# Kernel tuning notes

Measured on AMD Instinct MI355X. Metric: run time of the kernel, lower is better.

## Reference

```python
import jax, jax.numpy as jnp
import numpy as np

# dims
BB, T, D_IN = 16, 2048, 64
D = 512          # hidden_dim (d_model)
DI = 2 * D       # d_inner (expand=2)
N = 16           # d_state
DC = 4           # d_conv
R = D // 16      # dt_rank = 32
L = 3            # n_layer
D_OUT = 128


def setup_inputs() -> dict:
    key = jax.random.key(0)
    ks = jax.random.split(key, 10)
    g = lambda k, shape, s: (jax.random.normal(k, shape, jnp.float32) * s)
    A_log = jnp.tile(jnp.log(jnp.arange(1, N + 1, dtype=jnp.float32))[None, None, :], (L, DI, 1))
    return {
        "x": g(ks[0], (BB, T, D_IN), 1.0),
        "Wi": g(ks[1], (D, D_IN), 0.05), "bi": jnp.zeros((D,), jnp.float32),
        "Win": g(ks[2], (L, 2 * DI, D), 0.02),
        "convw": g(ks[3], (L, DI, DC), 0.2), "convb": jnp.zeros((L, DI), jnp.float32),
        "Wx": g(ks[4], (L, R + 2 * N, DI), 0.02),
        "Wdt": g(ks[5], (L, DI, R), 0.05), "bdt": jnp.full((L, DI), -1.0, jnp.float32),
        "A_log": A_log, "Dp": jnp.ones((L, DI), jnp.float32),
        "Wout": g(ks[6], (L, D, DI), 0.02),
        "Wo": g(ks[7], (D_OUT, D), 0.05), "bo": jnp.zeros((D_OUT,), jnp.float32),
    }


def _selective_scan(u, delta, A, Bm, Cm, Dv):
    # u, delta: [B,T,DI]; A: [DI,N]; Bm, Cm: [B,T,N]; Dv: [DI]
    def step(h, inp):
        d_t, u_t, B_t, C_t = inp  # [B,DI],[B,DI],[B,N],[B,N]
        dA = jnp.exp(d_t[:, :, None] * A)                      # [B,DI,N]
        h = dA * h + (d_t * u_t)[:, :, None] * B_t[:, None, :]  # [B,DI,N]
        y = jnp.einsum('bdn,bn->bd', h, C_t)
        return h, y

    h0 = jnp.zeros((u.shape[0], u.shape[2], A.shape[1]), u.dtype)
    xs = (delta.transpose(1, 0, 2), u.transpose(1, 0, 2),
          Bm.transpose(1, 0, 2), Cm.transpose(1, 0, 2))
    _, ys = jax.lax.scan(step, h0, xs)
    return ys.transpose(1, 0, 2) + u * Dv


def _mamba_layer(x, Win, cw, cb, Wx, Wdt, bdt, A_log, Dv, Wout):
    xz = x @ Win.T                      # [B,T,2*DI]
    xin, z = jnp.split(xz, 2, axis=-1)
    # causal depthwise conv1d
    xc = jax.lax.conv_general_dilated(
        xin.transpose(0, 2, 1), cw[:, None, :], (1,), [(DC - 1, 0)],
        feature_group_count=DI, dimension_numbers=('NCH', 'OIH', 'NCH'))
    u = jax.nn.silu((xc + cb[None, :, None]).transpose(0, 2, 1))  # [B,T,DI]
    dbc = u @ Wx.T                      # [B,T,R+2N]
    dt, Bm, Cm = dbc[..., :R], dbc[..., R:R + N], dbc[..., R + N:]
    delta = jax.nn.softplus(dt @ Wdt.T + bdt)
    A = -jnp.exp(A_log)
    y = _selective_scan(u, delta, A, Bm, Cm, Dv)
    return (y * jax.nn.silu(z)) @ Wout.T


def reference(x, Wi, bi, Win, convw, convb, Wx, Wdt, bdt, A_log, Dp, Wout, Wo, bo):
    h = x @ Wi.T + bi
    for l in range(L):
        h = _mamba_layer(h, Win[l], convw[l], convb[l], Wx[l], Wdt[l], bdt[l],
                         A_log[l], Dp[l], Wout[l])
    return jnp.tanh(h @ Wo.T + bo)  # [B,T,output_dim]
```

## Files before the change

kernel.cpp:

```cpp
#include <hip/hip_runtime.h>
#include <hip/hip_bf16.h>

#define BB_ 16
#define T_ 2048
#define DIN_ 64
#define D_ 512
#define DI_ 1024
#define N_ 16
#define DC_ 4
#define R_ 32
#define L_ 3
#define DOUT_ 128
#define CL_ 64
#define NCH_ (T_ / CL_)

typedef __attribute__((ext_vector_type(8))) _Float16 f16x8;
typedef __attribute__((ext_vector_type(4))) float f32x4;

__device__ __forceinline__ float silu_f(float x) { return x / (1.f + __expf(-x)); }

__device__ __forceinline__ float softplus_f(float t) {
    return fmaxf(t, 0.f) + __logf(1.f + __expf(-fabsf(t)));
}

__device__ __forceinline__ unsigned short f2h(float f) {
    union { _Float16 h; unsigned short u; } c;
    c.h = (_Float16)f;
    return c.u;
}

__device__ __forceinline__ void gload_lds16(const unsigned short* g,
                                            unsigned short* l) {
    __builtin_amdgcn_global_load_lds(
        (const __attribute__((address_space(1))) void*)g,
        (__attribute__((address_space(3))) void*)l, 16, 0, 0);
}

__device__ __forceinline__ float decode_scale(unsigned int bits) {
    if (bits == 0u) return 1.f;
    const int E = (int)(bits >> 23) & 0xFF;
    return __uint_as_float((unsigned)(265 - E) << 23);
}

__device__ __forceinline__ uint4 pack8(float4 lo, float4 hi, float s) {
    union { uint4 u; unsigned short h[8]; } r;
    r.h[0] = f2h(lo.x * s); r.h[1] = f2h(lo.y * s);
    r.h[2] = f2h(lo.z * s); r.h[3] = f2h(lo.w * s);
    r.h[4] = f2h(hi.x * s); r.h[5] = f2h(hi.y * s);
    r.h[6] = f2h(hi.z * s); r.h[7] = f2h(hi.w * s);
    return r.u;
}

__device__ __forceinline__ const float* wregion(
    int r, const float* Win, const float* Wout, const float* Wx,
    const float* Wdt, const float* Wo, size_t* n4)
{
    if (r < 3)       { *n4 = 262144; return Win  + (size_t)r * 1048576; }
    else if (r < 6)  { *n4 = 131072; return Wout + (size_t)(r - 3) * 524288; }
    else if (r == 6) { *n4 = 16384;  return Wo; }
    else if (r < 10) { *n4 = 16384;  return Wx  + (size_t)(r - 7) * 65536; }
    else             { *n4 = 8192;   return Wdt + (size_t)(r - 10) * 32768; }
}

__global__ __launch_bounds__(256) void amax_all(
    const float* __restrict__ Win, const float* __restrict__ Wout,
    const float* __restrict__ Wx, const float* __restrict__ Wdt,
    const float* __restrict__ Wo, unsigned int* __restrict__ scales)
{
    size_t n4;
    const float* p = wregion(blockIdx.z, Win, Wout, Wx, Wdt, Wo, &n4);
    float m = 0.f;
    for (size_t i = (size_t)blockIdx.x * 256 + threadIdx.x; i < n4;
         i += (size_t)gridDim.x * 256) {
        const float4 v = ((const float4*)p)[i];
        m = fmaxf(m, fmaxf(fmaxf(fabsf(v.x), fabsf(v.y)),
                           fmaxf(fabsf(v.z), fabsf(v.w))));
    }
#pragma unroll
    for (int off = 32; off; off >>= 1) m = fmaxf(m, __shfl_down(m, off));
    __shared__ float sm[4];
    if ((threadIdx.x & 63) == 0) sm[threadIdx.x >> 6] = m;
    __syncthreads();
    if (threadIdx.x == 0) {
        const float b = fmaxf(fmaxf(sm[0], sm[1]), fmaxf(sm[2], sm[3]));
        atomicMax(scales + blockIdx.z, __float_as_uint(b));
    }
}

__global__ __launch_bounds__(256) void cast_all(
    const float* __restrict__ Win, const float* __restrict__ Wout,
    const float* __restrict__ Wx, const float* __restrict__ Wdt,
    const float* __restrict__ Wo,
    unsigned short* __restrict__ WinH, unsigned short* __restrict__ WoutH,
    unsigned short* __restrict__ WxH, unsigned short* __restrict__ WdtH,
    unsigned short* __restrict__ WoH,
    const unsigned int* __restrict__ scales)
{
    const int r = blockIdx.z;
    size_t n4;
    const float* p = wregion(r, Win, Wout, Wx, Wdt, Wo, &n4);
    unsigned short* o;
    if (r < 3)       o = WinH  + (size_t)r * 1048576;
    else if (r < 6)  o = WoutH + (size_t)(r - 3) * 524288;
    else if (r == 6) o = WoH;
    else if (r < 10) o = WxH   + (size_t)(r - 7) * 65536;
    else             o = WdtH  + (size_t)(r - 10) * 32768;
    const float s = decode_scale(scales[r]);
    for (size_t i = (size_t)blockIdx.x * 256 + threadIdx.x; i < n4;
         i += (size_t)gridDim.x * 256) {
        const float4 v = ((const float4*)p)[i];
        ((ushort4*)o)[i] = make_ushort4(f2h(v.x * s), f2h(v.y * s),
                                        f2h(v.z * s), f2h(v.w * s));
    }
}

template<int ACT>
__global__ __launch_bounds__(256) void gemm_f32a_t128(
    const float* __restrict__ A, int lda,
    const unsigned short* __restrict__ B, int ldb,
    const float* __restrict__ bias,
    float* __restrict__ C, int ldc, int K,
    const unsigned int* __restrict__ sa, const unsigned int* __restrict__ sb,
    unsigned int* __restrict__ oamax)
{
    __shared__ __align__(16) unsigned short As[128 * 32];
    __shared__ __align__(16) unsigned short Bs[2][128 * 32];
    const int tid  = threadIdx.x;
    const int lane = tid & 63;
    const int w    = tid >> 6;
    const int wr   = (w >> 1) << 6;
    const int wc   = (w & 1) << 6;
    const int l15  = lane & 15, l4 = lane >> 4;
    const int row0 = blockIdx.y << 7, col0 = blockIdx.x << 7;
    const int tq   = tid >> 2;
    const int tr   = (tid & 3) << 3;

    const float sA  = decode_scale(*sa);
    const float inv = (1.f / sA) * (1.f / decode_scale(*sb));

    const float* Ar0 = A + (size_t)(row0 + tq) * lda + tr;
    const float* Ar1 = A + (size_t)(row0 + 64 + tq) * lda + tr;
    const unsigned short* Br0 = B + (size_t)(col0 + tq) * ldb + tr;
    const unsigned short* Br1 = B + (size_t)(col0 + 64 + tq) * ldb + tr;

    f32x4 acc[4][4];
#pragma unroll
    for (int m = 0; m < 4; ++m)
#pragma unroll
        for (int n = 0; n < 4; ++n) acc[m][n] = (f32x4){0.f, 0.f, 0.f, 0.f};

    float4 a0lo = *(const float4*)(Ar0), a0hi = *(const float4*)(Ar0 + 4);
    float4 a1lo = *(const float4*)(Ar1), a1hi = *(const float4*)(Ar1 + 4);
    gload_lds16(Br0, &Bs[0][tq * 32 + tr]);
    gload_lds16(Br1, &Bs[0][(64 + tq) * 32 + tr]);

    int cur = 0;
    for (int k0 = 0; k0 < K; k0 += 32) {
        __syncthreads();
        *(uint4*)&As[tq * 32 + tr]        = pack8(a0lo, a0hi, sA);
        *(uint4*)&As[(64 + tq) * 32 + tr] = pack8(a1lo, a1hi, sA);
        __syncthreads();

        if (k0 + 32 < K) {
            gload_lds16(Br0 + k0 + 32, &Bs[cur ^ 1][tq * 32 + tr]);
            gload_lds16(Br1 + k0 + 32, &Bs[cur ^ 1][(64 + tq) * 32 + tr]);
            a0lo = *(const float4*)(Ar0 + k0 + 32);
            a0hi = *(const float4*)(Ar0 + k0 + 36);
            a1lo = *(const float4*)(Ar1 + k0 + 32);
            a1hi = *(const float4*)(Ar1 + k0 + 36);
        }

        f16x8 af[4], bfr[4];
#pragma unroll
        for (int m = 0; m < 4; ++m)
            af[m] = *(const f16x8*)&As[(wr + m * 16 + l15) * 32 + l4 * 8];
#pragma unroll
        for (int n = 0; n < 4; ++n)
            bfr[n] = *(const f16x8*)&Bs[cur][(wc + n * 16 + l15) * 32 + l4 * 8];
#pragma unroll
        for (int m = 0; m < 4; ++m)
#pragma unroll
            for (int n = 0; n < 4; ++n)
                acc[m][n] = __builtin_amdgcn_mfma_f32_16x16x32_f16(
                    af[m], bfr[n], acc[m][n], 0, 0, 0);
        cur ^= 1;
    }

    float am = 0.f;
#pragma unroll
    for (int n = 0; n < 4; ++n) {
        const int col = col0 + wc + n * 16 + l15;
        float bc = 0.f;
        if (ACT == 3) bc = bias[col];
#pragma unroll
        for (int m = 0; m < 4; ++m) {
            const int rowb = row0 + wr + m * 16 + (l4 << 2);
#pragma unroll
            for (int r = 0; r < 4; ++r) {
                float v = acc[m][n][r] * inv;
                if (ACT == 3) v = tanhf(v + bc);
                C[(size_t)(rowb + r) * ldc + col] = v;
                am = fmaxf(am, fabsf(v));
            }
        }
    }
    if (oamax) {
#pragma unroll
        for (int off = 32; off; off >>= 1) am = fmaxf(am, __shfl_down(am, off));
        if (lane == 0) atomicMax(oamax, __float_as_uint(am));
    }
}

__global__ __launch_bounds__(256) void gemm_f16u_t64n(
    const float* __restrict__ A, int lda,
    const unsigned short* __restrict__ B, int ldb,
    float* __restrict__ C, int ldc, int K,
    const unsigned int* __restrict__ sa, const unsigned int* __restrict__ sb,
    unsigned int* __restrict__ dtmax)
{
    __shared__ __align__(16) unsigned short As[128 * 32];
    __shared__ __align__(16) unsigned short Bs[64 * 32];
    const int tid  = threadIdx.x;
    const int lane = tid & 63;
    const int w    = tid >> 6;
    const int l15  = lane & 15, l4 = lane >> 4;
    const int row0 = blockIdx.y << 7;
    const int tq   = tid >> 2;
    const int tr   = (tid & 3) << 3;

    const float sA  = decode_scale(*sa);
    const float inv = (1.f / sA) * (1.f / decode_scale(*sb));

    const float* Ar0 = A + (size_t)(row0 + tq) * lda + tr;
    const float* Ar1 = A + (size_t)(row0 + 64 + tq) * lda + tr;
    const unsigned short* Br = B + (size_t)tq * ldb + tr;

    f32x4 acc[2][4];
#pragma unroll
    for (int m = 0; m < 2; ++m)
#pragma unroll
        for (int n = 0; n < 4; ++n) acc[m][n] = (f32x4){0.f, 0.f, 0.f, 0.f};

    float4 a0lo = *(const float4*)(Ar0), a0hi = *(const float4*)(Ar0 + 4);
    float4 a1lo = *(const float4*)(Ar1), a1hi = *(const float4*)(Ar1 + 4);
    uint4  bv   = *(const uint4*)(Br);

    for (int k0 = 0; k0 < K; k0 += 32) {
        __syncthreads();
        *(uint4*)&As[tq * 32 + tr]        = pack8(a0lo, a0hi, sA);
        *(uint4*)&As[(64 + tq) * 32 + tr] = pack8(a1lo, a1hi, sA);
        *(uint4*)&Bs[tq * 32 + tr]        = bv;
        __syncthreads();

        if (k0 + 32 < K) {
            a0lo = *(const float4*)(Ar0 + k0 + 32);
            a0hi = *(const float4*)(Ar0 + k0 + 36);
            a1lo = *(const float4*)(Ar1 + k0 + 32);
            a1hi = *(const float4*)(Ar1 + k0 + 36);
            bv   = *(const uint4*)(Br  + k0 + 32);
        }

        f16x8 af[2], bfr[4];
#pragma unroll
        for (int m = 0; m < 2; ++m)
            af[m] = *(const f16x8*)&As[(w * 32 + m * 16 + l15) * 32 + l4 * 8];
#pragma unroll
        for (int n = 0; n < 4; ++n)
            bfr[n] = *(const f16x8*)&Bs[(n * 16 + l15) * 32 + l4 * 8];
#pragma unroll
        for (int m = 0; m < 2; ++m)
#pragma unroll
            for (int n = 0; n < 4; ++n)
                acc[m][n] = __builtin_amdgcn_mfma_f32_16x16x32_f16(
                    af[m], bfr[n], acc[m][n], 0, 0, 0);
    }

    float am = 0.f;
#pragma unroll
    for (int n = 0; n < 4; ++n) {
        const int col = n * 16 + l15;
#pragma unroll
        for (int m = 0; m < 2; ++m) {
            const int rowb = row0 + w * 32 + m * 16 + (l4 << 2);
#pragma unroll
            for (int r = 0; r < 4; ++r) {
                const float v = acc[m][n][r] * inv;
                C[(size_t)(rowb + r) * ldc + col] = v;
                if (n < 2) am = fmaxf(am, fabsf(v));
            }
        }
    }
#pragma unroll
    for (int off = 32; off; off >>= 1) am = fmaxf(am, __shfl_down(am, off));
    if (lane == 0) atomicMax(dtmax, __float_as_uint(am));
}

__global__ __launch_bounds__(256) void gemm_delta(
    const float* __restrict__ A,
    const unsigned short* __restrict__ B,
    const float* __restrict__ bias,
    float* __restrict__ C, int ldc,
    const unsigned int* __restrict__ sa, const unsigned int* __restrict__ sb)
{
    __shared__ __align__(16) unsigned short As[128 * 32];
    __shared__ __align__(16) unsigned short Bs[128 * 32];
    const int tid  = threadIdx.x;
    const int lane = tid & 63;
    const int w    = tid >> 6;
    const int wr   = (w >> 1) << 6;
    const int wc   = (w & 1) << 6;
    const int l15  = lane & 15, l4 = lane >> 4;
    const int row0 = blockIdx.y << 7, col0 = blockIdx.x << 7;
    const int tq   = tid >> 2;
    const int tr   = (tid & 3) << 3;

    const float sA  = decode_scale(*sa);
    const float inv = (1.f / sA) * (1.f / decode_scale(*sb));

    const float* Ar0 = A + (size_t)(row0 + tq) * 64 + tr;
    const float* Ar1 = A + (size_t)(row0 + 64 + tq) * 64 + tr;
    const float4 a0lo = *(const float4*)(Ar0), a0hi = *(const float4*)(Ar0 + 4);
    const float4 a1lo = *(const float4*)(Ar1), a1hi = *(const float4*)(Ar1 + 4);
    const uint4 bv0 = *(const uint4*)(B + (size_t)(col0 + tq) * 32 + tr);
    const uint4 bv1 = *(const uint4*)(B + (size_t)(col0 + 64 + tq) * 32 + tr);

    *(uint4*)&As[tq * 32 + tr]        = pack8(a0lo, a0hi, sA);
    *(uint4*)&As[(64 + tq) * 32 + tr] = pack8(a1lo, a1hi, sA);
    *(uint4*)&Bs[tq * 32 + tr]        = bv0;
    *(uint4*)&Bs[(64 + tq) * 32 + tr] = bv1;
    __syncthreads();

    f32x4 acc[4][4];
#pragma unroll
    for (int m = 0; m < 4; ++m)
#pragma unroll
        for (int n = 0; n < 4; ++n) acc[m][n] = (f32x4){0.f, 0.f, 0.f, 0.f};

    f16x8 af[4], bfr[4];
#pragma unroll
    for (int m = 0; m < 4; ++m)
        af[m] = *(const f16x8*)&As[(wr + m * 16 + l15) * 32 + l4 * 8];
#pragma unroll
    for (int n = 0; n < 4; ++n)
        bfr[n] = *(const f16x8*)&Bs[(wc + n * 16 + l15) * 32 + l4 * 8];
#pragma unroll
    for (int m = 0; m < 4; ++m)
#pragma unroll
        for (int n = 0; n < 4; ++n)
            acc[m][n] = __builtin_amdgcn_mfma_f32_16x16x32_f16(
                af[m], bfr[n], acc[m][n], 0, 0, 0);

#pragma unroll
    for (int n = 0; n < 4; ++n) {
        const int col = col0 + wc + n * 16 + l15;
        const float bc = bias[col];
#pragma unroll
        for (int m = 0; m < 4; ++m) {
            const int rowb = row0 + wr + m * 16 + (l4 << 2);
#pragma unroll
            for (int r = 0; r < 4; ++r) {
                const float t = acc[m][n][r] * inv + bc;
                C[(size_t)(rowb + r) * ldc + col] = softplus_f(t);
            }
        }
    }
}

__global__ __launch_bounds__(256) void gemm_in(
    const float* __restrict__ A, int lda,
    const float* __restrict__ B, int ldb,
    const float* __restrict__ bias,
    float* __restrict__ C, int ldc, int K,
    unsigned int* __restrict__ oamax)
{
    __shared__ __align__(16) float As[8][128];
    __shared__ __align__(16) float Bs[8][128];
    const int tid  = threadIdx.x;
    const int row0 = blockIdx.y << 7;
    const int col0 = blockIdx.x << 7;
    const int tx = tid & 15, ty = tid >> 4;

    float acc[8][8];
#pragma unroll
    for (int i = 0; i < 8; ++i)
#pragma unroll
        for (int j = 0; j < 8; ++j) acc[i][j] = 0.f;

    const int arow = tid >> 1;
    const int acol = (tid & 1) << 2;
    const float* Ap = A + (size_t)(row0 + arow) * lda + acol;
    const float* Bp = B + (size_t)(col0 + arow) * ldb + acol;

    for (int k0 = 0; k0 < K; k0 += 8) {
        const float4 av = *(const float4*)(Ap + k0);
        const float4 bv = *(const float4*)(Bp + k0);
        __syncthreads();
        As[acol + 0][arow] = av.x; As[acol + 1][arow] = av.y;
        As[acol + 2][arow] = av.z; As[acol + 3][arow] = av.w;
        Bs[acol + 0][arow] = bv.x; Bs[acol + 1][arow] = bv.y;
        Bs[acol + 2][arow] = bv.z; Bs[acol + 3][arow] = bv.w;
        __syncthreads();
#pragma unroll
        for (int k = 0; k < 8; ++k) {
            float a[8], b[8];
            *(float4*)&a[0] = *(const float4*)&As[k][ty << 3];
            *(float4*)&a[4] = *(const float4*)&As[k][(ty << 3) + 4];
            *(float4*)&b[0] = *(const float4*)&Bs[k][tx << 3];
            *(float4*)&b[4] = *(const float4*)&Bs[k][(tx << 3) + 4];
#pragma unroll
            for (int i = 0; i < 8; ++i)
#pragma unroll
                for (int j = 0; j < 8; ++j)
                    acc[i][j] = fmaf(a[i], b[j], acc[i][j]);
        }
    }

    float bv8[8];
#pragma unroll
    for (int j = 0; j < 8; ++j) bv8[j] = bias[col0 + (tx << 3) + j];

    float am = 0.f;
#pragma unroll
    for (int i = 0; i < 8; ++i) {
        float v[8];
#pragma unroll
        for (int j = 0; j < 8; ++j) {
            v[j] = acc[i][j] + bv8[j];
            am = fmaxf(am, fabsf(v[j]));
        }
        float* Cp = C + (size_t)(row0 + (ty << 3) + i) * ldc + col0 + (tx << 3);
        *(float4*)(Cp)     = make_float4(v[0], v[1], v[2], v[3]);
        *(float4*)(Cp + 4) = make_float4(v[4], v[5], v[6], v[7]);
    }
#pragma unroll
    for (int off = 32; off; off >>= 1) am = fmaxf(am, __shfl_down(am, off));
    if ((tid & 63) == 0) atomicMax(oamax, __float_as_uint(am));
}

__global__ __launch_bounds__(256) void conv_silu_kernel(
    const float* __restrict__ xz, const float* __restrict__ cw,
    const float* __restrict__ cb, float* __restrict__ u,
    size_t total4, unsigned int* __restrict__ uamax)
{
    float am = 0.f;
    for (size_t i = (size_t)blockIdx.x * 256 + threadIdx.x; i < total4;
         i += (size_t)gridDim.x * 256) {
        const size_t e = i * 4;
        const int c = (int)(e & (DI_ - 1));
        const size_t m = e >> 10;
        const int t = (int)(m & (T_ - 1));
        const float* xr = xz + m * 2048 + c;
        const float4 zero = make_float4(0.f, 0.f, 0.f, 0.f);
        const float4 x0 = (t >= 3) ? *(const float4*)(xr - 3 * 2048) : zero;
        const float4 x1 = (t >= 2) ? *(const float4*)(xr - 2 * 2048) : zero;
        const float4 x2 = (t >= 1) ? *(const float4*)(xr - 1 * 2048) : zero;
        const float4 x3 = *(const float4*)(xr);
        const float4 cbv = *(const float4*)(cb + c);
        const float4 w0 = *(const float4*)(cw + (size_t)c * 4);
        const float4 w1 = *(const float4*)(cw + (size_t)(c + 1) * 4);
        const float4 w2 = *(const float4*)(cw + (size_t)(c + 2) * 4);
        const float4 w3 = *(const float4*)(cw + (size_t)(c + 3) * 4);
        float4 r;
        r.x = silu_f(fmaf(x3.x, w0.w, fmaf(x2.x, w0.z, fmaf(x1.x, w0.y, fmaf(x0.x, w0.x, cbv.x)))));
        r.y = silu_f(fmaf(x3.y, w1.w, fmaf(x2.y, w1.z, fmaf(x1.y, w1.y, fmaf(x0.y, w1.x, cbv.y)))));
        r.z = silu_f(fmaf(x3.z, w2.w, fmaf(x2.z, w2.z, fmaf(x1.z, w2.y, fmaf(x0.z, w2.x, cbv.z)))));
        r.w = silu_f(fmaf(x3.w, w3.w, fmaf(x2.w, w3.z, fmaf(x1.w, w3.y, fmaf(x0.w, w3.x, cbv.w)))));
        *(float4*)(u + e) = r;
        am = fmaxf(am, fmaxf(fmaxf(fabsf(r.x), fabsf(r.y)),
                             fmaxf(fabsf(r.z), fabsf(r.w))));
    }
#pragma unroll
    for (int off = 32; off; off >>= 1) am = fmaxf(am, __shfl_down(am, off));
    __shared__ float sm[4];
    if ((threadIdx.x & 63) == 0) sm[threadIdx.x >> 6] = am;
    __syncthreads();
    if (threadIdx.x == 0) {
        const float b = fmaxf(fmaxf(sm[0], sm[1]), fmaxf(sm[2], sm[3]));
        atomicMax(uamax, __float_as_uint(b));
    }
}


__device__ __forceinline__ bool geo_check(const float* a2) {
    bool ok = true;
#pragma unroll
    for (int n = 1; n < N_; ++n)
        ok = ok && (fabsf(a2[n] - a2[0] * (n + 1)) <=
                    1e-5f * fmaxf(1.f, fabsf(a2[n])));
    return ok;
}

__global__ __launch_bounds__(256) void scan_pass1(
    const float* __restrict__ xz, const float* __restrict__ u,
    const float* __restrict__ dbc, const float* __restrict__ A_log_l,
    float* __restrict__ P, float* __restrict__ S)
{
    __shared__ float sB[CL_][N_];
    const int tid = threadIdx.x;
    const int b = blockIdx.x, ch = blockIdx.z;
    const int d = (blockIdx.y << 8) + tid;

    float a2[N_], Pm[N_], hs[N_];
#pragma unroll
    for (int n = 0; n < N_; ++n) {
        a2[n] = -__expf(A_log_l[d * N_ + n]) * 1.44269504f;
        Pm[n] = 1.f; hs[n] = 0.f;
    }
    const bool geo = geo_check(a2);
    for (int i = tid; i < CL_ * N_; i += 256) {
        const int tl = i >> 4, n = i & 15;
        sB[tl][n] = dbc[((size_t)b * T_ + ch * CL_ + tl) * 64 + 32 + n];
    }
    __syncthreads();

    if (geo) {
        for (int tt = 0; tt < CL_; ++tt) {
            const size_t m = (size_t)b * T_ + ch * CL_ + tt;
            const float dl = xz[m * 2048 + d];
            const float du = dl * u[m * DI_ + d];
            const float r = exp2f(dl * a2[0]);
            float dA = r;
#pragma unroll
            for (int n = 0; n < N_; ++n) {
                Pm[n] *= dA;
                hs[n] = fmaf(dA, hs[n], du * sB[tt][n]);
                dA *= r;
            }
        }
    } else {
        for (int tt = 0; tt < CL_; ++tt) {
            const size_t m = (size_t)b * T_ + ch * CL_ + tt;
            const float dl = xz[m * 2048 + d];
            const float du = dl * u[m * DI_ + d];
#pragma unroll
            for (int n = 0; n < N_; ++n) {
                const float dA = exp2f(dl * a2[n]);
                Pm[n] *= dA;
                hs[n] = fmaf(dA, hs[n], du * sB[tt][n]);
            }
        }
    }
#pragma unroll
    for (int n = 0; n < N_; ++n) {
        const size_t idx = (size_t)(((b * NCH_ + ch) * N_ + n) << 10) + d;
        P[idx] = Pm[n]; S[idx] = hs[n];
    }
}

__global__ __launch_bounds__(256) void scan_carry(
    const float* __restrict__ P, float* __restrict__ S)
{
    const size_t gid = (size_t)blockIdx.x * 256 + threadIdx.x;
    const int d = (int)(gid & 1023);
    const int n = (int)((gid >> 10) & 15);
    const int b = (int)(gid >> 14);
    float hc = 0.f;
    for (int ch = 0; ch < NCH_; ++ch) {
        const size_t idx = (size_t)(((b * NCH_ + ch) * N_ + n) << 10) + d;
        const float p = P[idx], s = S[idx];
        S[idx] = hc;
        hc = fmaf(p, hc, s);
    }
}

__global__ __launch_bounds__(256) void scan_pass3(
    float* __restrict__ xz, const float* __restrict__ u,
    const float* __restrict__ dbc, const float* __restrict__ A_log_l,
    const float* __restrict__ Dp_l, const float* __restrict__ S,
    unsigned int* __restrict__ gmax)
{
    __shared__ float sB[CL_][N_];
    __shared__ float sC[CL_][N_];
    const int tid = threadIdx.x;
    const int b = blockIdx.x, ch = blockIdx.z;
    const int d = (blockIdx.y << 8) + tid;

    float a2[N_], hs[N_];
#pragma unroll
    for (int n = 0; n < N_; ++n) {
        a2[n] = -__expf(A_log_l[d * N_ + n]) * 1.44269504f;
        hs[n] = S[(size_t)(((b * NCH_ + ch) * N_ + n) << 10) + d];
    }
    const bool geo = geo_check(a2);
    const float Dpd = Dp_l[d];
    for (int i = tid; i < CL_ * N_; i += 256) {
        const int tl = i >> 4, n = i & 15;
        const size_t base = ((size_t)b * T_ + ch * CL_ + tl) * 64;
        sB[tl][n] = dbc[base + 32 + n];
        sC[tl][n] = dbc[base + 48 + n];
    }
    __syncthreads();

    float gm = 0.f;
    if (geo) {
        for (int tt = 0; tt < CL_; ++tt) {
            const size_t m = (size_t)b * T_ + ch * CL_ + tt;
            const float dl = xz[m * 2048 + d];
            const float uv = u[m * DI_ + d];
            const float du = dl * uv;
            const float r = exp2f(dl * a2[0]);
            float dA = r;
            float yv = 0.f;
#pragma unroll
            for (int n = 0; n < N_; ++n) {
                hs[n] = fmaf(dA, hs[n], du * sB[tt][n]);
                yv = fmaf(hs[n], sC[tt][n], yv);
                dA *= r;
            }
            yv = fmaf(uv, Dpd, yv);
            const float g = yv * silu_f(xz[m * 2048 + DI_ + d]);
            xz[m * 2048 + d] = g;
            gm = fmaxf(gm, fabsf(g));
        }
    } else {
        for (int tt = 0; tt < CL_; ++tt) {
            const size_t m = (size_t)b * T_ + ch * CL_ + tt;
            const float dl = xz[m * 2048 + d];
            const float uv = u[m * DI_ + d];
            const float du = dl * uv;
            float yv = 0.f;
#pragma unroll
            for (int n = 0; n < N_; ++n) {
                const float dA = exp2f(dl * a2[n]);
                hs[n] = fmaf(dA, hs[n], du * sB[tt][n]);
                yv = fmaf(hs[n], sC[tt][n], yv);
            }
            yv = fmaf(uv, Dpd, yv);
            const float g = yv * silu_f(xz[m * 2048 + DI_ + d]);
            xz[m * 2048 + d] = g;
            gm = fmaxf(gm, fabsf(g));
        }
    }
#pragma unroll
    for (int off = 32; off; off >>= 1) gm = fmaxf(gm, __shfl_down(gm, off));
    if ((tid & 63) == 0) atomicMax(gmax, __float_as_uint(gm));
}

extern "C" void kernel_launch(void* const* d_in, const int* in_sizes, int n_in,
                              void* d_out, int out_size, void* d_ws, size_t ws_size,
                              hipStream_t stream) {
    const float* x     = (const float*)d_in[0];
    const float* Wi    = (const float*)d_in[1];
    const float* bi    = (const float*)d_in[2];
    const float* Win   = (const float*)d_in[3];
    const float* convw = (const float*)d_in[4];
    const float* convb = (const float*)d_in[5];
    const float* Wx    = (const float*)d_in[6];
    const float* Wdt   = (const float*)d_in[7];
    const float* bdt   = (const float*)d_in[8];
    const float* A_log = (const float*)d_in[9];
    const float* Dp    = (const float*)d_in[10];
    const float* Wout  = (const float*)d_in[11];
    const float* Wo    = (const float*)d_in[12];
    const float* bo    = (const float*)d_in[13];
    float* out = (float*)d_out;

    const size_t rowf = 3648;
    const size_t wextra =
        (3 * 1048576 + 3 * 524288 + 65536 + 3 * 65536 + 3 * 32768) / 2 + 32;
    int CB = BB_;
    while (CB > 1 && ((size_t)CB * T_ * rowf + wextra) * sizeof(float) > ws_size) CB >>= 1;
    const size_t Mc = (size_t)CB * T_;

    const dim3 blk(256);
    const int rowTiles = (int)(Mc / 128);

    float* ws   = (float*)d_ws;
    float* xz   = ws;
    float* u    = xz + Mc * 2048;
    float* dbc  = u  + Mc * 1024;
    float* hPS  = dbc + Mc * 64;
    float* hb   = hPS;
    float* Pbuf = hPS;
    float* Sbuf = hPS + (size_t)CB * NCH_ * N_ * DI_;
    unsigned short* WinH  = (unsigned short*)(hPS + Mc * 512);
    unsigned short* WoutH = WinH + 3 * 1048576;
    unsigned short* WoH   = WoutH + 3 * 524288;
    unsigned short* WxH   = WoH + 65536;
    unsigned short* WdtH  = WxH + 3 * 65536;
    unsigned int* scales  = (unsigned int*)(WdtH + 3 * 32768);

    hipMemsetAsync(scales, 0, 32 * sizeof(unsigned int), stream);

    amax_all<<<dim3(128, 1, 13), blk, 0, stream>>>(Win, Wout, Wx, Wdt, Wo, scales);
    cast_all<<<dim3(64, 1, 13), blk, 0, stream>>>(
        Win, Wout, Wx, Wdt, Wo, WinH, WoutH, WxH, WdtH, WoH, scales);

    for (int c = 0; c < BB_ / CB; ++c) {
        const float* x_c = x + (size_t)c * Mc * DIN_;
        float* out_c     = out + (size_t)c * Mc * DOUT_;

        hipMemsetAsync(scales + 13, 0, 13 * sizeof(unsigned int), stream);

        gemm_in<<<dim3(D_ / 128, rowTiles), blk, 0, stream>>>(
            x_c, DIN_, Wi, DIN_, bi, hb, D_, DIN_, scales + 13);

        for (int l = 0; l < L_; ++l) {
            const float* cw_l   = convw + (size_t)l * DI_ * DC_;
            const float* cb_l   = convb + (size_t)l * DI_;
            const float* bdt_l  = bdt  + (size_t)l * DI_;
            const float* Alog_l = A_log + (size_t)l * DI_ * N_;
            const float* Dp_l   = Dp   + (size_t)l * DI_;

            gemm_f32a_t128<0><<<dim3(2048 / 128, rowTiles), blk, 0, stream>>>(
                hb, D_, WinH + (size_t)l * 1048576, D_, nullptr,
                xz, 2048, D_, scales + 13 + l, scales + l, nullptr);

            conv_silu_kernel<<<dim3(2048), blk, 0, stream>>>(
                xz, cw_l, cb_l, u, Mc * DI_ / 4, scales + 20 + l);

            gemm_f16u_t64n<<<dim3(1, rowTiles), blk, 0, stream>>>(
                u, DI_, WxH + (size_t)l * 65536, DI_, dbc, 64, DI_,
                scales + 20 + l, scales + 7 + l, scales + 23 + l);

            gemm_delta<<<dim3(DI_ / 128, rowTiles), blk, 0, stream>>>(
                dbc, WdtH + (size_t)l * 32768, bdt_l, xz, 2048,
                scales + 23 + l, scales + 10 + l);

            scan_pass1<<<dim3(CB, DI_ / 256, NCH_), blk, 0, stream>>>(
                xz, u, dbc, Alog_l, Pbuf, Sbuf);
            scan_carry<<<dim3(CB * 64), blk, 0, stream>>>(Pbuf, Sbuf);
            scan_pass3<<<dim3(CB, DI_ / 256, NCH_), blk, 0, stream>>>(
                xz, u, dbc, Alog_l, Dp_l, Sbuf, scales + 17 + l);

            gemm_f32a_t128<0><<<dim3(D_ / 128, rowTiles), blk, 0, stream>>>(
                xz, 2048, WoutH + (size_t)l * 524288, DI_, nullptr,
                hb, D_, DI_, scales + 17 + l, scales + 3 + l, scales + 14 + l);
        }

        gemm_f32a_t128<3><<<dim3(DOUT_ / 128, rowTiles), blk, 0, stream>>>(
            hb, D_, WoH, D_, bo, out_c, DOUT_, D_,
            scales + 16, scales + 6, nullptr);
    }
}
```

Measured before the change: 2.670 ms.

## Fuse dt projection and softplus into scan passes, drop gemm_delta kernel

```diff
diff --git a/kernel.cpp b/kernel.cpp
--- a/kernel.cpp
+++ b/kernel.cpp
@@ -53,22 +53,21 @@
 
 __device__ __forceinline__ const float* wregion(
     int r, const float* Win, const float* Wout, const float* Wx,
-    const float* Wdt, const float* Wo, size_t* n4)
+    const float* Wo, size_t* n4)
 {
     if (r < 3)       { *n4 = 262144; return Win  + (size_t)r * 1048576; }
     else if (r < 6)  { *n4 = 131072; return Wout + (size_t)(r - 3) * 524288; }
     else if (r == 6) { *n4 = 16384;  return Wo; }
-    else if (r < 10) { *n4 = 16384;  return Wx  + (size_t)(r - 7) * 65536; }
-    else             { *n4 = 8192;   return Wdt + (size_t)(r - 10) * 32768; }
+    else             { *n4 = 16384;  return Wx  + (size_t)(r - 7) * 65536; }
 }
 
 __global__ __launch_bounds__(256) void amax_all(
     const float* __restrict__ Win, const float* __restrict__ Wout,
-    const float* __restrict__ Wx, const float* __restrict__ Wdt,
-    const float* __restrict__ Wo, unsigned int* __restrict__ scales)
+    const float* __restrict__ Wx, const float* __restrict__ Wo,
+    unsigned int* __restrict__ scales)
 {
     size_t n4;
-    const float* p = wregion(blockIdx.z, Win, Wout, Wx, Wdt, Wo, &n4);
+    const float* p = wregion(blockIdx.z, Win, Wout, Wx, Wo, &n4);
     float m = 0.f;
     for (size_t i = (size_t)blockIdx.x * 256 + threadIdx.x; i < n4;
          i += (size_t)gridDim.x * 256) {
@@ -89,22 +88,19 @@
 
 __global__ __launch_bounds__(256) void cast_all(
     const float* __restrict__ Win, const float* __restrict__ Wout,
-    const float* __restrict__ Wx, const float* __restrict__ Wdt,
-    const float* __restrict__ Wo,
+    const float* __restrict__ Wx, const float* __restrict__ Wo,
     unsigned short* __restrict__ WinH, unsigned short* __restrict__ WoutH,
-    unsigned short* __restrict__ WxH, unsigned short* __restrict__ WdtH,
-    unsigned short* __restrict__ WoH,
+    unsigned short* __restrict__ WxH, unsigned short* __restrict__ WoH,
     const unsigned int* __restrict__ scales)
 {
     const int r = blockIdx.z;
     size_t n4;
-    const float* p = wregion(r, Win, Wout, Wx, Wdt, Wo, &n4);
+    const float* p = wregion(r, Win, Wout, Wx, Wo, &n4);
     unsigned short* o;
     if (r < 3)       o = WinH  + (size_t)r * 1048576;
     else if (r < 6)  o = WoutH + (size_t)(r - 3) * 524288;
     else if (r == 6) o = WoH;
-    else if (r < 10) o = WxH   + (size_t)(r - 7) * 65536;
-    else             o = WdtH  + (size_t)(r - 10) * 32768;
+    else             o = WxH   + (size_t)(r - 7) * 65536;
     const float s = decode_scale(scales[r]);
     for (size_t i = (size_t)blockIdx.x * 256 + threadIdx.x; i < n4;
          i += (size_t)gridDim.x * 256) {
@@ -215,8 +211,7 @@
     const float* __restrict__ A, int lda,
     const unsigned short* __restrict__ B, int ldb,
     float* __restrict__ C, int ldc, int K,
-    const unsigned int* __restrict__ sa, const unsigned int* __restrict__ sb,
-    unsigned int* __restrict__ dtmax)
+    const unsigned int* __restrict__ sa, const unsigned int* __restrict__ sb)
 {
     __shared__ __align__(16) unsigned short As[128 * 32];
     __shared__ __align__(16) unsigned short Bs[64 * 32];
@@ -275,7 +270,6 @@
                     af[m], bfr[n], acc[m][n], 0, 0, 0);
     }
 
-    float am = 0.f;
 #pragma unroll
     for (int n = 0; n < 4; ++n) {
         const int col = n * 16 + l15;
@@ -283,85 +277,8 @@
         for (int m = 0; m < 2; ++m) {
             const int rowb = row0 + w * 32 + m * 16 + (l4 << 2);
 #pragma unroll
-            for (int r = 0; r < 4; ++r) {
-                const float v = acc[m][n][r] * inv;
-                C[(size_t)(rowb + r) * ldc + col] = v;
-                if (n < 2) am = fmaxf(am, fabsf(v));
-            }
-        }
-    }
-#pragma unroll
-    for (int off = 32; off; off >>= 1) am = fmaxf(am, __shfl_down(am, off));
-    if (lane == 0) atomicMax(dtmax, __float_as_uint(am));
-}
-
-__global__ __launch_bounds__(256) void gemm_delta(
-    const float* __restrict__ A,
-    const unsigned short* __restrict__ B,
-    const float* __restrict__ bias,
-    float* __restrict__ C, int ldc,
-    const unsigned int* __restrict__ sa, const unsigned int* __restrict__ sb)
-{
-    __shared__ __align__(16) unsigned short As[128 * 32];
-    __shared__ __align__(16) unsigned short Bs[128 * 32];
-    const int tid  = threadIdx.x;
-    const int lane = tid & 63;
-    const int w    = tid >> 6;
-    const int wr   = (w >> 1) << 6;
-    const int wc   = (w & 1) << 6;
-    const int l15  = lane & 15, l4 = lane >> 4;
-    const int row0 = blockIdx.y << 7, col0 = blockIdx.x << 7;
-    const int tq   = tid >> 2;
-    const int tr   = (tid & 3) << 3;
-
-    const float sA  = decode_scale(*sa);
-    const float inv = (1.f / sA) * (1.f / decode_scale(*sb));
-
-    const float* Ar0 = A + (size_t)(row0 + tq) * 64 + tr;
-    const float* Ar1 = A + (size_t)(row0 + 64 + tq) * 64 + tr;
-    const float4 a0lo = *(const float4*)(Ar0), a0hi = *(const float4*)(Ar0 + 4);
-    const float4 a1lo = *(const float4*)(Ar1), a1hi = *(const float4*)(Ar1 + 4);
-    const uint4 bv0 = *(const uint4*)(B + (size_t)(col0 + tq) * 32 + tr);
-    const uint4 bv1 = *(const uint4*)(B + (size_t)(col0 + 64 + tq) * 32 + tr);
-
-    *(uint4*)&As[tq * 32 + tr]        = pack8(a0lo, a0hi, sA);
-    *(uint4*)&As[(64 + tq) * 32 + tr] = pack8(a1lo, a1hi, sA);
-    *(uint4*)&Bs[tq * 32 + tr]        = bv0;
-    *(uint4*)&Bs[(64 + tq) * 32 + tr] = bv1;
-    __syncthreads();
-
-    f32x4 acc[4][4];
-#pragma unroll
-    for (int m = 0; m < 4; ++m)
-#pragma unroll
-        for (int n = 0; n < 4; ++n) acc[m][n] = (f32x4){0.f, 0.f, 0.f, 0.f};
-
-    f16x8 af[4], bfr[4];
-#pragma unroll
-    for (int m = 0; m < 4; ++m)
-        af[m] = *(const f16x8*)&As[(wr + m * 16 + l15) * 32 + l4 * 8];
-#pragma unroll
-    for (int n = 0; n < 4; ++n)
-        bfr[n] = *(const f16x8*)&Bs[(wc + n * 16 + l15) * 32 + l4 * 8];
-#pragma unroll
-    for (int m = 0; m < 4; ++m)
-#pragma unroll
-        for (int n = 0; n < 4; ++n)
-            acc[m][n] = __builtin_amdgcn_mfma_f32_16x16x32_f16(
-                af[m], bfr[n], acc[m][n], 0, 0, 0);
-
-#pragma unroll
-    for (int n = 0; n < 4; ++n) {
-        const int col = col0 + wc + n * 16 + l15;
-        const float bc = bias[col];
-#pragma unroll
-        for (int m = 0; m < 4; ++m) {
-            const int rowb = row0 + wr + m * 16 + (l4 << 2);
-#pragma unroll
-            for (int r = 0; r < 4; ++r) {
-                const float t = acc[m][n][r] * inv + bc;
-                C[(size_t)(rowb + r) * ldc + col] = softplus_f(t);
-            }
+            for (int r = 0; r < 4; ++r)
+                C[(size_t)(rowb + r) * ldc + col] = acc[m][n][r] * inv;
         }
     }
 }
@@ -491,59 +408,85 @@
 }
 
 __global__ __launch_bounds__(256) void scan_pass1(
-    const float* __restrict__ xz, const float* __restrict__ u,
-    const float* __restrict__ dbc, const float* __restrict__ A_log_l,
+    const float* __restrict__ u, const float* __restrict__ dbc,
+    const float* __restrict__ A_log_l, const float* __restrict__ Wdt_l,
+    const float* __restrict__ bdt_l,
     float* __restrict__ P, float* __restrict__ S)
 {
-    __shared__ float sB[CL_][N_];
+    __shared__ __align__(16) float sAll[CL_][64];
     const int tid = threadIdx.x;
     const int b = blockIdx.x, ch = blockIdx.z;
     const int d = (blockIdx.y << 8) + tid;
 
-    float a2[N_], Pm[N_], hs[N_];
+    float a2[N_], hs[N_];
 #pragma unroll
     for (int n = 0; n < N_; ++n) {
         a2[n] = -__expf(A_log_l[d * N_ + n]) * 1.44269504f;
-        Pm[n] = 1.f; hs[n] = 0.f;
+        hs[n] = 0.f;
     }
     const bool geo = geo_check(a2);
-    for (int i = tid; i < CL_ * N_; i += 256) {
-        const int tl = i >> 4, n = i & 15;
-        sB[tl][n] = dbc[((size_t)b * T_ + ch * CL_ + tl) * 64 + 32 + n];
-    }
+    float wdt[32];
+#pragma unroll
+    for (int k = 0; k < 32; k += 4)
+        *(float4*)&wdt[k] = *(const float4*)(Wdt_l + (size_t)d * 32 + k);
+    const float bdt_d = bdt_l[d];
+
+    const size_t base64 = ((size_t)b * T_ + (size_t)ch * CL_) * 64;
+    float* sflat = &sAll[0][0];
+    for (int i = tid; i < CL_ * 64; i += 256) sflat[i] = dbc[base64 + i];
     __syncthreads();
 
+    float sdl = 0.f;
     if (geo) {
         for (int tt = 0; tt < CL_; ++tt) {
+            float t = bdt_d;
+#pragma unroll
+            for (int k = 0; k < 32; k += 4) {
+                const float4 dv = *(const float4*)&sAll[tt][k];
+                t = fmaf(dv.x, wdt[k + 0], t);
+                t = fmaf(dv.y, wdt[k + 1], t);
+                t = fmaf(dv.z, wdt[k + 2], t);
+                t = fmaf(dv.w, wdt[k + 3], t);
+            }
+            const float dl = softplus_f(t);
+            sdl += dl;
             const size_t m = (size_t)b * T_ + ch * CL_ + tt;
-            const float dl = xz[m * 2048 + d];
             const float du = dl * u[m * DI_ + d];
             const float r = exp2f(dl * a2[0]);
             float dA = r;
 #pragma unroll
             for (int n = 0; n < N_; ++n) {
-                Pm[n] *= dA;
-                hs[n] = fmaf(dA, hs[n], du * sB[tt][n]);
+                hs[n] = fmaf(dA, hs[n], du * sAll[tt][32 + n]);
                 dA *= r;
             }
         }
     } else {
         for (int tt = 0; tt < CL_; ++tt) {
+            float t = bdt_d;
+#pragma unroll
+            for (int k = 0; k < 32; k += 4) {
+                const float4 dv = *(const float4*)&sAll[tt][k];
+                t = fmaf(dv.x, wdt[k + 0], t);
+                t = fmaf(dv.y, wdt[k + 1], t);
+                t = fmaf(dv.z, wdt[k + 2], t);
+                t = fmaf(dv.w, wdt[k + 3], t);
+            }
+            const float dl = softplus_f(t);
+            sdl += dl;
             const size_t m = (size_t)b * T_ + ch * CL_ + tt;
-            const float dl = xz[m * 2048 + d];
             const float du = dl * u[m * DI_ + d];
 #pragma unroll
             for (int n = 0; n < N_; ++n) {
                 const float dA = exp2f(dl * a2[n]);
-                Pm[n] *= dA;
-                hs[n] = fmaf(dA, hs[n], du * sB[tt][n]);
+                hs[n] = fmaf(dA, hs[n], du * sAll[tt][32 + n]);
             }
         }
     }
 #pragma unroll
     for (int n = 0; n < N_; ++n) {
         const size_t idx = (size_t)(((b * NCH_ + ch) * N_ + n) << 10) + d;
-        P[idx] = Pm[n]; S[idx] = hs[n];
+        P[idx] = exp2f(sdl * a2[n]);
+        S[idx] = hs[n];
     }
 }
 
@@ -566,11 +509,11 @@
 __global__ __launch_bounds__(256) void scan_pass3(
     float* __restrict__ xz, const float* __restrict__ u,
     const float* __restrict__ dbc, const float* __restrict__ A_log_l,
+    const float* __restrict__ Wdt_l, const float* __restrict__ bdt_l,
     const float* __restrict__ Dp_l, const float* __restrict__ S,
     unsigned int* __restrict__ gmax)
 {
-    __shared__ float sB[CL_][N_];
-    __shared__ float sC[CL_][N_];
+    __shared__ __align__(16) float sAll[CL_][64];
     const int tid = threadIdx.x;
     const int b = blockIdx.x, ch = blockIdx.z;
     const int d = (blockIdx.y << 8) + tid;
@@ -582,20 +525,32 @@
         hs[n] = S[(size_t)(((b * NCH_ + ch) * N_ + n) << 10) + d];
     }
     const bool geo = geo_check(a2);
+    float wdt[32];
+#pragma unroll
+    for (int k = 0; k < 32; k += 4)
+        *(float4*)&wdt[k] = *(const float4*)(Wdt_l + (size_t)d * 32 + k);
+    const float bdt_d = bdt_l[d];
     const float Dpd = Dp_l[d];
-    for (int i = tid; i < CL_ * N_; i += 256) {
-        const int tl = i >> 4, n = i & 15;
-        const size_t base = ((size_t)b * T_ + ch * CL_ + tl) * 64;
-        sB[tl][n] = dbc[base + 32 + n];
-        sC[tl][n] = dbc[base + 48 + n];
-    }
+
+    const size_t base64 = ((size_t)b * T_ + (size_t)ch * CL_) * 64;
+    float* sflat = &sAll[0][0];
+    for (int i = tid; i < CL_ * 64; i += 256) sflat[i] = dbc[base64 + i];
     __syncthreads();
 
     float gm = 0.f;
     if (geo) {
         for (int tt = 0; tt < CL_; ++tt) {
+            float t = bdt_d;
+#pragma unroll
+            for (int k = 0; k < 32; k += 4) {
+                const float4 dv = *(const float4*)&sAll[tt][k];
+                t = fmaf(dv.x, wdt[k + 0], t);
+                t = fmaf(dv.y, wdt[k + 1], t);
+                t = fmaf(dv.z, wdt[k + 2], t);
+                t = fmaf(dv.w, wdt[k + 3], t);
+            }
+            const float dl = softplus_f(t);
             const size_t m = (size_t)b * T_ + ch * CL_ + tt;
-            const float dl = xz[m * 2048 + d];
             const float uv = u[m * DI_ + d];
             const float du = dl * uv;
             const float r = exp2f(dl * a2[0]);
@@ -603,8 +558,8 @@
             float yv = 0.f;
 #pragma unroll
             for (int n = 0; n < N_; ++n) {
-                hs[n] = fmaf(dA, hs[n], du * sB[tt][n]);
-                yv = fmaf(hs[n], sC[tt][n], yv);
+                hs[n] = fmaf(dA, hs[n], du * sAll[tt][32 + n]);
+                yv = fmaf(hs[n], sAll[tt][48 + n], yv);
                 dA *= r;
             }
             yv = fmaf(uv, Dpd, yv);
@@ -614,16 +569,25 @@
         }
     } else {
         for (int tt = 0; tt < CL_; ++tt) {
+            float t = bdt_d;
+#pragma unroll
+            for (int k = 0; k < 32; k += 4) {
+                const float4 dv = *(const float4*)&sAll[tt][k];
+                t = fmaf(dv.x, wdt[k + 0], t);
+                t = fmaf(dv.y, wdt[k + 1], t);
+                t = fmaf(dv.z, wdt[k + 2], t);
+                t = fmaf(dv.w, wdt[k + 3], t);
+            }
+            const float dl = softplus_f(t);
             const size_t m = (size_t)b * T_ + ch * CL_ + tt;
-            const float dl = xz[m * 2048 + d];
             const float uv = u[m * DI_ + d];
             const float du = dl * uv;
             float yv = 0.f;
 #pragma unroll
             for (int n = 0; n < N_; ++n) {
                 const float dA = exp2f(dl * a2[n]);
-                hs[n] = fmaf(dA, hs[n], du * sB[tt][n]);
-                yv = fmaf(hs[n], sC[tt][n], yv);
+                hs[n] = fmaf(dA, hs[n], du * sAll[tt][32 + n]);
+                yv = fmaf(hs[n], sAll[tt][48 + n], yv);
             }
             yv = fmaf(uv, Dpd, yv);
             const float g = yv * silu_f(xz[m * 2048 + DI_ + d]);
@@ -657,7 +621,7 @@
 
     const size_t rowf = 3648;
     const size_t wextra =
-        (3 * 1048576 + 3 * 524288 + 65536 + 3 * 65536 + 3 * 32768) / 2 + 32;
+        (3 * 1048576 + 3 * 524288 + 65536 + 3 * 65536) / 2 + 32;
     int CB = BB_;
     while (CB > 1 && ((size_t)CB * T_ * rowf + wextra) * sizeof(float) > ws_size) CB >>= 1;
     const size_t Mc = (size_t)CB * T_;
@@ -677,59 +641,55 @@
     unsigned short* WoutH = WinH + 3 * 1048576;
     unsigned short* WoH   = WoutH + 3 * 524288;
     unsigned short* WxH   = WoH + 65536;
-    unsigned short* WdtH  = WxH + 3 * 65536;
-    unsigned int* scales  = (unsigned int*)(WdtH + 3 * 32768);
+    unsigned int* scales  = (unsigned int*)(WxH + 3 * 65536);
 
     hipMemsetAsync(scales, 0, 32 * sizeof(unsigned int), stream);
 
-    amax_all<<<dim3(128, 1, 13), blk, 0, stream>>>(Win, Wout, Wx, Wdt, Wo, scales);
-    cast_all<<<dim3(64, 1, 13), blk, 0, stream>>>(
-        Win, Wout, Wx, Wdt, Wo, WinH, WoutH, WxH, WdtH, WoH, scales);
+    amax_all<<<dim3(128, 1, 10), blk, 0, stream>>>(Win, Wout, Wx, Wo, scales);
+    cast_all<<<dim3(64, 1, 10), blk, 0, stream>>>(
+        Win, Wout, Wx, Wo, WinH, WoutH, WxH, WoH, scales);
 
     for (int c = 0; c < BB_ / CB; ++c) {
         const float* x_c = x + (size_t)c * Mc * DIN_;
         float* out_c     = out + (size_t)c * Mc * DOUT_;
 
-        hipMemsetAsync(scales + 13, 0, 13 * sizeof(unsigned int), stream);
+        hipMemsetAsync(scales + 10, 0, 10 * sizeof(unsigned int), stream);
 
         gemm_in<<<dim3(D_ / 128, rowTiles), blk, 0, stream>>>(
-            x_c, DIN_, Wi, DIN_, bi, hb, D_, DIN_, scales + 13);
+            x_c, DIN_, Wi, DIN_, bi, hb, D_, DIN_, scales + 10);
 
         for (int l = 0; l < L_; ++l) {
             const float* cw_l   = convw + (size_t)l * DI_ * DC_;
             const float* cb_l   = convb + (size_t)l * DI_;
+            const float* Wdt_l  = Wdt  + (size_t)l * DI_ * R_;
             const float* bdt_l  = bdt  + (size_t)l * DI_;
             const float* Alog_l = A_log + (size_t)l * DI_ * N_;
             const float* Dp_l   = Dp   + (size_t)l * DI_;
 
             gemm_f32a_t128<0><<<dim3(2048 / 128, rowTiles), blk, 0, stream>>>(
                 hb, D_, WinH + (size_t)l * 1048576, D_, nullptr,
-                xz, 2048, D_, scales + 13 + l, scales + l, nullptr);
+                xz, 2048, D_, scales + 10 + l, scales + l, nullptr);
 
             conv_silu_kernel<<<dim3(2048), blk, 0, stream>>>(
-                xz, cw_l, cb_l, u, Mc * DI_ / 4, scales + 20 + l);
+                xz, cw_l, cb_l, u, Mc * DI_ / 4, scales + 17 + l);
 
             gemm_f16u_t64n<<<dim3(1, rowTiles), blk, 0, stream>>>(
                 u, DI_, WxH + (size_t)l * 65536, DI_, dbc, 64, DI_,
-                scales + 20 + l, scales + 7 + l, scales + 23 + l);
-
-            gemm_delta<<<dim3(DI_ / 128, rowTiles), blk, 0, stream>>>(
-                dbc, WdtH + (size_t)l * 32768, bdt_l, xz, 2048,
-                scales + 23 + l, scales + 10 + l);
+                scales + 17 + l, scales + 7 + l);
 
             scan_pass1<<<dim3(CB, DI_ / 256, NCH_), blk, 0, stream>>>(
-                xz, u, dbc, Alog_l, Pbuf, Sbuf);
+                u, dbc, Alog_l, Wdt_l, bdt_l, Pbuf, Sbuf);
             scan_carry<<<dim3(CB * 64), blk, 0, stream>>>(Pbuf, Sbuf);
             scan_pass3<<<dim3(CB, DI_ / 256, NCH_), blk, 0, stream>>>(
-                xz, u, dbc, Alog_l, Dp_l, Sbuf, scales + 17 + l);
+                xz, u, dbc, Alog_l, Wdt_l, bdt_l, Dp_l, Sbuf, scales + 14 + l);
 
             gemm_f32a_t128<0><<<dim3(D_ / 128, rowTiles), blk, 0, stream>>>(
                 xz, 2048, WoutH + (size_t)l * 524288, DI_, nullptr,
-                hb, D_, DI_, scales + 17 + l, scales + 3 + l, scales + 14 + l);
+                hb, D_, DI_, scales + 14 + l, scales + 3 + l, scales + 11 + l);
         }
 
         gemm_f32a_t128<3><<<dim3(DOUT_ / 128, rowTiles), blk, 0, stream>>>(
             hb, D_, WoH, D_, bo, out_c, DOUT_, D_,
-            scales + 16, scales + 6, nullptr);
-    }
-}
+            scales + 13, scales + 6, nullptr);
+    }
+}
```

New measurement: 2.594 ms. 1.03x faster.
